# Kernel tuning notes

Measured on AMD Instinct MI355X. Metric: run time of the kernel, lower is better.

Reference implementation:

```python
import jax, jax.numpy as jnp
import numpy as np

T = 2048
HID = 4096
H = 32
HKV = 8
D = 128
EPS = 1e-5
THETA = 1e6
WINDOW = 1024


def setup_inputs() -> dict:
    key = jax.random.key(0)
    k1, k2, k3 = jax.random.split(key, 3)
    return {
        "positions": jnp.arange(T, dtype=jnp.int32),
        "hidden_states": jax.random.normal(k1, (T, HID), dtype=jnp.float32),
        "w_qkv": jax.random.normal(k2, (HID, (H + 2 * HKV) * D), dtype=jnp.float32) * 0.02,
        "q_norm_w": jnp.ones((D,), dtype=jnp.float32),
        "k_norm_w": jnp.ones((D,), dtype=jnp.float32),
        "w_o": jax.random.normal(k3, (H * D, HID), dtype=jnp.float32) * 0.02,
    }


def _rmsnorm(x, w):
    # per-head RMSNorm over last dim (head_dim)
    var = jnp.mean(x * x, axis=-1, keepdims=True)
    return x * jax.lax.rsqrt(var + EPS) * w


def _rope_neox(x, positions):
    # x: [T, heads, D]; neox style: rotate halves
    half = D // 2
    inv_freq = 1.0 / (THETA ** (jnp.arange(0, half, dtype=jnp.float32) / half))
    ang = positions.astype(jnp.float32)[:, None] * inv_freq  # [T, half]
    cos = jnp.cos(ang)[:, None, :]
    sin = jnp.sin(ang)[:, None, :]
    x1, x2 = x[..., :half], x[..., half:]
    return jnp.concatenate([x1 * cos - x2 * sin, x2 * cos + x1 * sin], axis=-1)


def reference(positions, hidden_states, w_qkv, q_norm_w, k_norm_w, w_o):
    qkv = hidden_states @ w_qkv  # [T, (H+2Hkv)*D]
    q, k, v = jnp.split(qkv, [H * D, (H + HKV) * D], axis=-1)
    q = _rmsnorm(q.reshape(T, H, D), q_norm_w)
    k = _rmsnorm(k.reshape(T, HKV, D), k_norm_w)
    v = v.reshape(T, HKV, D)

    q = _rope_neox(q, positions)
    k = _rope_neox(k, positions)

    # GQA: expand kv heads to H
    rep = H // HKV
    k = jnp.repeat(k, rep, axis=1)  # [T, H, D]
    v = jnp.repeat(v, rep, axis=1)

    scale = D ** -0.5
    scores = jnp.einsum('thd,shd->hts', q, k) * scale  # [H, T, T]
    i = jnp.arange(T)[:, None]
    j = jnp.arange(T)[None, :]
    mask = (j <= i) & (i - j < WINDOW)  # causal + sliding window
    scores = jnp.where(mask[None], scores, -jnp.inf)
    probs = jax.nn.softmax(scores, axis=-1)
    attn = jnp.einsum('hts,shd->thd', probs, v).reshape(T, H * D)
    return attn @ w_o
```

## Files before the change

kernel.cpp:

```cpp
#include <hip/hip_runtime.h>
#include <hip/hip_bf16.h>
#include <stdint.h>

#define T_SEQ  2048
#define HIDDEN 4096
#define NHEAD  32
#define NKV    8
#define HDIM   128
#define NQKV   6144
#define WINDOW 1024
#define SCALE  0.08838834764831845f
#define SHIFT  12.0f

typedef __attribute__((ext_vector_type(8))) short          short8;
typedef __attribute__((ext_vector_type(8))) unsigned short ushort8_t;
typedef __attribute__((ext_vector_type(4))) float          floatx4;

__device__ __forceinline__ unsigned short f2bf(float f) {
    union { float f; unsigned int u; } v; v.f = f;
    unsigned int u = v.u;
    unsigned int r = (u + 0x7FFFu + ((u >> 16) & 1u)) >> 16;
    return (unsigned short)r;
}
__device__ __forceinline__ float bf2f(unsigned short u) {
    union { unsigned int u; float f; } v; v.u = ((unsigned int)u) << 16;
    return v.f;
}

#define GLOBAL_AS(p) ((const __attribute__((address_space(1))) void*)(p))
#define LDS_AS(p)    ((__attribute__((address_space(3))) void*)(p))

#define S_BARRIER() do { asm volatile("" ::: "memory");  \
                         __builtin_amdgcn_s_barrier();   \
                         asm volatile("" ::: "memory"); } while (0)

__global__ __launch_bounds__(256) void convert_bf16_kernel(
        const float* __restrict__ X, unsigned short* __restrict__ Y, int n4) {
    int i = blockIdx.x * blockDim.x + threadIdx.x;
    if (i < n4) {
        float4 v = ((const float4*)X)[i];
        ushort4 o;
        o.x = f2bf(v.x); o.y = f2bf(v.y); o.z = f2bf(v.z); o.w = f2bf(v.w);
        ((ushort4*)Y)[i] = o;
    }
}

__global__ __launch_bounds__(256) void transpose_bf16_kernel(
        const float* __restrict__ W, unsigned short* __restrict__ Wt, int K, int N) {
    __shared__ float tile[128][33];
    const int n0 = blockIdx.x * 32, k0 = blockIdx.y * 128;
    const int tid = threadIdx.x;
    const int rr = tid >> 3, cc = tid & 7;
    #pragma unroll
    for (int p = 0; p < 4; ++p) {
        int r = p * 32 + rr;
        float4 v = *(const float4*)&W[(size_t)(k0 + r) * N + n0 + cc * 4];
        tile[r][cc * 4 + 0] = v.x; tile[r][cc * 4 + 1] = v.y;
        tile[r][cc * 4 + 2] = v.z; tile[r][cc * 4 + 3] = v.w;
    }
    __syncthreads();
    const int nL = tid >> 3, kc = tid & 7;
    #pragma unroll
    for (int q = 0; q < 2; ++q) {
        int kbase = kc * 8 + q * 64;
        ushort8_t o;
        #pragma unroll
        for (int j = 0; j < 8; ++j) o[j] = f2bf(tile[kbase + j][nL]);
        *(ushort8_t*)&Wt[(size_t)(n0 + nL) * K + k0 + kbase] = o;
    }
}

#define STG3_A(bufi, kt, r)                                                       \
    __builtin_amdgcn_global_load_lds(                                             \
        GLOBAL_AS(A + (size_t)(m0 + rRow[r]) * K + ((kt) << 6) + rOff[r]),        \
        LDS_AS(&As3[bufi][((r) * 256 + tid) * 8]), 16, 0, 0)
#define STG3_B(bufi, kt, r)                                                       \
    __builtin_amdgcn_global_load_lds(                                             \
        GLOBAL_AS(B + (size_t)(n0 + rRow[r]) * K + ((kt) << 6) + rOff[r]),        \
        LDS_AS(&Bs3[bufi][((r) * 256 + tid) * 8]), 16, 0, 0)

template <bool BF16_OUT>
__global__ __launch_bounds__(256, 2) void gemm_bt3_kernel(
        const unsigned short* __restrict__ A,
        const unsigned short* __restrict__ B,
        void* __restrict__ Cv, int M, int N, int K) {
    __shared__ __align__(16) unsigned short As3[2][128 * 64];
    __shared__ __align__(16) unsigned short Bs3[2][128 * 64];

    const int tid  = threadIdx.x;
    const int lane = tid & 63, wave = tid >> 6;
    const int wr = wave >> 1, wc = wave & 1;
    const int lrow = lane & 15, hi = lane >> 4;

    const int nwg = gridDim.x * gridDim.y;
    int wg = blockIdx.y * gridDim.x + blockIdx.x;
    wg = (wg & 7) * (nwg >> 3) + (wg >> 3);
    const int bx = wg % gridDim.x;
    const int by = wg / gridDim.x;
    const int m0 = by * 128, n0 = bx * 128;

    const int NT = K >> 6;

    int rRow[4], rOff[4];
    #pragma unroll
    for (int r = 0; r < 4; ++r) {
        int idx = r * 256 + tid;
        int row = idx >> 3;
        rRow[r] = row;
        rOff[r] = ((idx & 7) ^ (row & 7)) * 8;
    }

    const int sA0   = (hi ^ (lrow & 7)) * 8;
    const int aBase = (wr * 64 + lrow) * 64;
    const int bBase = (wc * 64 + lrow) * 64;

    floatx4 acc[4][4] = {};

    auto compute_tile = [&](int cur) {
        const unsigned short* ap = &As3[cur][0];
        const unsigned short* bp = &Bs3[cur][0];
        short8 af[4][2], bf[4][2];
        #pragma unroll
        for (int m = 0; m < 4; ++m)
            #pragma unroll
            for (int kh = 0; kh < 2; ++kh)
                af[m][kh] = *(const short8*)(ap + aBase + m * 1024 + (sA0 ^ (kh << 5)));
        #pragma unroll
        for (int n = 0; n < 4; ++n)
            #pragma unroll
            for (int kh = 0; kh < 2; ++kh)
                bf[n][kh] = *(const short8*)(bp + bBase + n * 1024 + (sA0 ^ (kh << 5)));
        __builtin_amdgcn_s_setprio(1);
        #pragma unroll
        for (int m = 0; m < 4; ++m)
            #pragma unroll
            for (int n = 0; n < 4; ++n) {
                acc[m][n] = __builtin_amdgcn_mfma_f32_16x16x32_bf16(
                    af[m][0], bf[n][0], acc[m][n], 0, 0, 0);
                acc[m][n] = __builtin_amdgcn_mfma_f32_16x16x32_bf16(
                    af[m][1], bf[n][1], acc[m][n], 0, 0, 0);
            }
        __builtin_amdgcn_s_setprio(0);
    };

    #pragma unroll
    for (int r = 0; r < 4; ++r) STG3_A(0, 0, r);
    #pragma unroll
    for (int r = 0; r < 4; ++r) STG3_B(0, 0, r);
    asm volatile("s_waitcnt vmcnt(0)" ::: "memory");
    S_BARRIER();

    for (int t = 0; t < NT - 1; ++t) {
        const int cur = t & 1;
        #pragma unroll
        for (int r = 0; r < 4; ++r) STG3_A(cur ^ 1, t + 1, r);
        #pragma unroll
        for (int r = 0; r < 4; ++r) STG3_B(cur ^ 1, t + 1, r);
        compute_tile(cur);
        asm volatile("s_waitcnt vmcnt(0)" ::: "memory");
        S_BARRIER();
    }
    compute_tile((NT - 1) & 1);

    const int rowb = hi * 4, col = lrow;
    #pragma unroll
    for (int mi = 0; mi < 4; ++mi)
        #pragma unroll
        for (int ni = 0; ni < 4; ++ni) {
            size_t base = (size_t)(m0 + wr * 64 + mi * 16 + rowb) * N
                        + (n0 + wc * 64 + ni * 16 + col);
            #pragma unroll
            for (int r = 0; r < 4; ++r) {
                if (BF16_OUT)
                    ((unsigned short*)Cv)[base + (size_t)r * N] = f2bf(acc[mi][ni][r]);
                else
                    ((float*)Cv)[base + (size_t)r * N] = acc[mi][ni][r];
            }
        }
}

#define STG4_A(bufi, kt, r)                                                       \
    __builtin_amdgcn_global_load_lds(                                             \
        GLOBAL_AS(A + (size_t)(m0 + rRowA[r]) * K + ((kt) << 6) + rOffA[r]),      \
        LDS_AS(&As4[bufi][((r) * 256 + tid) * 8]), 16, 0, 0)
#define STG4_B(bufi, kt, r)                                                       \
    __builtin_amdgcn_global_load_lds(                                             \
        GLOBAL_AS(B + (size_t)(n0 + rRowB[r]) * K + ((kt) << 6) + rOffB[r]),      \
        LDS_AS(&Bs4[bufi][((r) * 256 + tid) * 8]), 16, 0, 0)

template <bool BF16_OUT>
__global__ __launch_bounds__(256, 2) void gemm_bt4_kernel(
        const unsigned short* __restrict__ A,
        const unsigned short* __restrict__ B,
        void* __restrict__ Cv, int M, int N, int K) {
    __shared__ __align__(16) unsigned short As4[2][128 * 64];
    __shared__ __align__(16) unsigned short Bs4[2][192 * 64];

    const int tid  = threadIdx.x;
    const int lane = tid & 63, wave = tid >> 6;
    const int wr = wave >> 1, wc = wave & 1;
    const int lrow = lane & 15, hi = lane >> 4;

    const int nwg = gridDim.x * gridDim.y;
    int wg = blockIdx.y * gridDim.x + blockIdx.x;
    wg = (wg & 7) * (nwg >> 3) + (wg >> 3);
    const int by = wg % gridDim.x;
    const int bx = wg / gridDim.x;
    const int m0 = by * 128, n0 = bx * 192;

    const int NT = K >> 6;

    int rRowA[4], rOffA[4];
    #pragma unroll
    for (int r = 0; r < 4; ++r) {
        int idx = r * 256 + tid;
        int row = idx >> 3;
        rRowA[r] = row;
        rOffA[r] = ((idx & 7) ^ (row & 7)) * 8;
    }
    int rRowB[6], rOffB[6];
    #pragma unroll
    for (int r = 0; r < 6; ++r) {
        int idx = r * 256 + tid;
        int row = idx >> 3;
        rRowB[r] = row;
        rOffB[r] = ((idx & 7) ^ (row & 7)) * 8;
    }

    const int sA0   = (hi ^ (lrow & 7)) * 8;
    const int aBase = (wr * 64 + lrow) * 64;
    const int bBase = (wc * 96 + lrow) * 64;

    floatx4 acc[4][6] = {};

    auto compute_tile = [&](int cur) {
        const unsigned short* ap = &As4[cur][0];
        const unsigned short* bp = &Bs4[cur][0];
        short8 af[4][2], bf[6][2];
        #pragma unroll
        for (int m = 0; m < 4; ++m)
            #pragma unroll
            for (int kh = 0; kh < 2; ++kh)
                af[m][kh] = *(const short8*)(ap + aBase + m * 1024 + (sA0 ^ (kh << 5)));
        #pragma unroll
        for (int n = 0; n < 6; ++n)
            #pragma unroll
            for (int kh = 0; kh < 2; ++kh)
                bf[n][kh] = *(const short8*)(bp + bBase + n * 1024 + (sA0 ^ (kh << 5)));
        __builtin_amdgcn_s_setprio(1);
        #pragma unroll
        for (int m = 0; m < 4; ++m)
            #pragma unroll
            for (int n = 0; n < 6; ++n) {
                acc[m][n] = __builtin_amdgcn_mfma_f32_16x16x32_bf16(
                    af[m][0], bf[n][0], acc[m][n], 0, 0, 0);
                acc[m][n] = __builtin_amdgcn_mfma_f32_16x16x32_bf16(
                    af[m][1], bf[n][1], acc[m][n], 0, 0, 0);
            }
        __builtin_amdgcn_s_setprio(0);
    };

    #pragma unroll
    for (int r = 0; r < 4; ++r) STG4_A(0, 0, r);
    #pragma unroll
    for (int r = 0; r < 6; ++r) STG4_B(0, 0, r);
    asm volatile("s_waitcnt vmcnt(0)" ::: "memory");
    S_BARRIER();

    for (int t = 0; t < NT - 1; ++t) {
        const int cur = t & 1;
        #pragma unroll
        for (int r = 0; r < 4; ++r) STG4_A(cur ^ 1, t + 1, r);
        #pragma unroll
        for (int r = 0; r < 6; ++r) STG4_B(cur ^ 1, t + 1, r);
        compute_tile(cur);
        asm volatile("s_waitcnt vmcnt(0)" ::: "memory");
        S_BARRIER();
    }
    compute_tile((NT - 1) & 1);

    const int rowb = hi * 4, col = lrow;
    #pragma unroll
    for (int mi = 0; mi < 4; ++mi)
        #pragma unroll
        for (int ni = 0; ni < 6; ++ni) {
            size_t base = (size_t)(m0 + wr * 64 + mi * 16 + rowb) * N
                        + (n0 + wc * 96 + ni * 16 + col);
            #pragma unroll
            for (int r = 0; r < 4; ++r) {
                if (BF16_OUT)
                    ((unsigned short*)Cv)[base + (size_t)r * N] = f2bf(acc[mi][ni][r]);
                else
                    ((float*)Cv)[base + (size_t)r * N] = acc[mi][ni][r];
            }
        }
}

__global__ __launch_bounds__(256) void rope_table_kernel(
        const int* __restrict__ positions, float2* __restrict__ rope) {
    int idx = blockIdx.x * 256 + threadIdx.x;
    int t = idx >> 6, i = idx & 63;
    float inv_freq = expf((float)i * -0.2158673524681918f);
    float sn, cs;
    sincosf((float)positions[t] * inv_freq, &sn, &cs);
    rope[idx] = make_float2(cs, sn);
}

__global__ __launch_bounds__(256) void qkv_post_kernel(
        const unsigned short* __restrict__ qkv, const float2* __restrict__ rope,
        const float* __restrict__ qw, const float* __restrict__ kw,
        unsigned short* __restrict__ qb,
        unsigned short* __restrict__ kb,
        unsigned short* __restrict__ vbT) {
    const int head = blockIdx.y;
    const int t0   = blockIdx.x * 32;
    const int tid  = threadIdx.x;

    if (head < 40) {
        const int r  = tid >> 3;
        const int q8 = tid & 7;
        const int t  = t0 + r;
        const unsigned short* src = qkv + (size_t)t * NQKV
                         + (head < 32 ? head * 128 : 4096 + (head - 32) * 128)
                         + q8 * 16;
        const float* w = (head < 32) ? qw : kw;

        ushort8_t u0 = *(const ushort8_t*)src;
        ushort8_t u1 = *(const ushort8_t*)(src + 8);
        float x[16];
        #pragma unroll
        for (int j = 0; j < 8; ++j) { x[j] = bf2f(u0[j]); x[8 + j] = bf2f(u1[j]); }

        float ss = 0.f;
        #pragma unroll
        for (int j = 0; j < 16; ++j) ss = fmaf(x[j], x[j], ss);
        ss += __shfl_xor(ss, 1); ss += __shfl_xor(ss, 2); ss += __shfl_xor(ss, 4);
        float sc = rsqrtf(ss * (1.f / 128.f) + 1e-5f);

        float xn[16], xp[16];
        #pragma unroll
        for (int j = 0; j < 16; ++j) xn[j] = x[j] * sc * w[q8 * 16 + j];
        #pragma unroll
        for (int j = 0; j < 16; ++j) xp[j] = __shfl_xor(xn[j], 4);

        const float2* rp = rope + (size_t)t * 64 + (q8 & 3) * 16;
        ushort8_t o0, o1;
        #pragma unroll
        for (int j = 0; j < 8; ++j) {
            float2 cs = rp[j];
            float res = (q8 < 4) ? (xn[j] * cs.x - xp[j] * cs.y)
                                 : (xn[j] * cs.x + xp[j] * cs.y);
            o0[j] = f2bf(res);
        }
        #pragma unroll
        for (int j = 0; j < 8; ++j) {
            float2 cs = rp[8 + j];
            float res = (q8 < 4) ? (xn[8+j] * cs.x - xp[8+j] * cs.y)
                                 : (xn[8+j] * cs.x + xp[8+j] * cs.y);
            o1[j] = f2bf(res);
        }
        unsigned short* dst = (head < 32)
            ? qb + ((size_t)t * 32 + head) * 128 + q8 * 16
            : kb + ((size_t)t * 8 + (head - 32)) * 128 + q8 * 16;
        *(ushort8_t*)dst       = o0;
        *(ushort8_t*)(dst + 8) = o1;
    } else {
        __shared__ float tile[128][33];
        const int hk = head - 40;
        {
            const int r = tid >> 3, c8 = tid & 7;
            const unsigned short* src =
                qkv + (size_t)(t0 + r) * NQKV + 5120 + hk * 128 + c8 * 16;
            ushort8_t u0 = *(const ushort8_t*)src;
            ushort8_t u1 = *(const ushort8_t*)(src + 8);
            #pragma unroll
            for (int j = 0; j < 8; ++j) {
                tile[c8 * 16 + j][r]     = bf2f(u0[j]);
                tile[c8 * 16 + 8 + j][r] = bf2f(u1[j]);
            }
        }
        __syncthreads();
        {
            const int d = tid >> 1, th = tid & 1;
            ushort8_t o0, o1;
            #pragma unroll
            for (int j = 0; j < 8; ++j) o0[j] = f2bf(tile[d][th * 16 + j]);
            #pragma unroll
            for (int j = 0; j < 8; ++j) o1[j] = f2bf(tile[d][th * 16 + 8 + j]);
            unsigned short* dst = vbT + ((size_t)hk * 128 + d) * T_SEQ + t0 + th * 16;
            *(ushort8_t*)dst       = o0;
            *(ushort8_t*)(dst + 8) = o1;
        }
    }
}

__global__ __launch_bounds__(256) void attention_kernel(
        const unsigned short* __restrict__ qb,
        const unsigned short* __restrict__ kb,
        const unsigned short* __restrict__ vbT,
        unsigned short* __restrict__ attnb) {
    const int h    = blockIdx.x & 31;
    const int Q0   = (blockIdx.x >> 5) * 64;
    const int tid  = threadIdx.x, wave = tid >> 6, lane = tid & 63;
    const int keyA = lane & 15, g = lane >> 4;
    const int hk   = h >> 2;
    const int qlo  = Q0 + wave * 16;

    __shared__ __align__(16) unsigned short ks [2][32 * 128];
    __shared__ __align__(16) unsigned short vsT[2][128 * 32];
    __shared__ __align__(16) unsigned short Pa [4 * 16 * 40];

    unsigned short* pw = Pa + wave * 640;

    int kRow[2], kOff[2], vD[2], vOff[2];
    #pragma unroll
    for (int i = 0; i < 2; ++i) {
        int c = i * 256 + tid;
        {   int row = c >> 4, u = c & 15;
            kRow[i] = row; kOff[i] = (u ^ (row & 7)) * 8; }
        {   int d = c >> 2, u = c & 3;
            vD[i] = d; vOff[i] = (u ^ (d & 3)) * 8; }
    }

    auto stage = [&](int buf, int s0) {
        #pragma unroll
        for (int i = 0; i < 2; ++i) {
            int c = i * 256 + tid;
            const unsigned short* kp =
                kb + ((size_t)(s0 + kRow[i]) * 8 + hk) * 128 + kOff[i];
            __builtin_amdgcn_global_load_lds(GLOBAL_AS(kp),
                LDS_AS(&ks[buf][c * 8]), 16, 0, 0);
            const unsigned short* vp =
                vbT + ((size_t)hk * 128 + vD[i]) * T_SEQ + s0 + vOff[i];
            __builtin_amdgcn_global_load_lds(GLOBAL_AS(vp),
                LDS_AS(&vsT[buf][c * 8]), 16, 0, 0);
        }
    };

    short8 qa[4];
    {
        const unsigned short* qp = qb + ((size_t)(qlo + keyA) * 32 + h) * 128 + g * 8;
        #pragma unroll
        for (int s = 0; s < 4; ++s) qa[s] = *(const short8*)(qp + s * 32);
    }

    floatx4 acc[8] = {};
    float l_part[4] = {0.f, 0.f, 0.f, 0.f};

    const int s_begin = (Q0 >= WINDOW) ? ((Q0 - (WINDOW - 1)) & ~31) : 0;
    const int s_end   = Q0 + 63;

    stage(0, s_begin);
    asm volatile("s_waitcnt vmcnt(0)" ::: "memory");
    S_BARRIER();

    int cur = 0;
    for (int s0 = s_begin; s0 <= s_end; s0 += 32) {
        if (s0 + 32 <= s_end) stage(cur ^ 1, s0 + 32);

        if (s0 <= qlo + 15 && s0 + 31 >= qlo - (WINDOW - 1)) {
            const unsigned short* ksb  = &ks[cur][0];
            const unsigned short* vsb  = &vsT[cur][0];
            floatx4 sa0 = {}, sa1 = {};
            #pragma unroll
            for (int kst = 0; kst < 4; ++kst) {
                int u = g + 4 * kst;
                short8 k0 = *(const short8*)(ksb + keyA * 128 + (u ^ (keyA & 7)) * 8);
                short8 k1 = *(const short8*)(ksb + (16 + keyA) * 128 + (u ^ ((16 + keyA) & 7)) * 8);
                sa0 = __builtin_amdgcn_mfma_f32_16x16x32_bf16(qa[kst], k0, sa0, 0, 0, 0);
                sa1 = __builtin_amdgcn_mfma_f32_16x16x32_bf16(qa[kst], k1, sa1, 0, 0, 0);
            }
            float p0[4], p1[4];
            #pragma unroll
            for (int r = 0; r < 4; ++r) {
                int row = qlo + 4 * g + r;
                int sA = s0 + keyA, sB = sA + 16;
                bool vA = (sA <= row) && (row - sA < WINDOW);
                bool vB = (sB <= row) && (row - sB < WINDOW);
                p0[r] = vA ? __expf(fmaf(sa0[r], SCALE, -SHIFT)) : 0.f;
                p1[r] = vB ? __expf(fmaf(sa1[r], SCALE, -SHIFT)) : 0.f;
                l_part[r] += p0[r] + p1[r];
            }
            #pragma unroll
            for (int r = 0; r < 4; ++r) {
                pw[(4 * g + r) * 40 + keyA]      = f2bf(p0[r]);
                pw[(4 * g + r) * 40 + keyA + 16] = f2bf(p1[r]);
            }
            short8 pf = *(const short8*)(pw + keyA * 40 + g * 8);

            #pragma unroll
            for (int t = 0; t < 8; ++t) {
                int d = t * 16 + keyA;
                short8 vf = *(const short8*)(vsb + d * 32 + (g ^ (d & 3)) * 8);
                acc[t] = __builtin_amdgcn_mfma_f32_16x16x32_bf16(pf, vf, acc[t], 0, 0, 0);
            }
        }
        asm volatile("s_waitcnt vmcnt(0)" ::: "memory");
        S_BARRIER();
        cur ^= 1;
    }

    float inv[4];
    #pragma unroll
    for (int r = 0; r < 4; ++r) {
        float l = l_part[r];
        l += __shfl_xor(l, 1); l += __shfl_xor(l, 2);
        l += __shfl_xor(l, 4); l += __shfl_xor(l, 8);
        inv[r] = 1.f / l;
    }
    #pragma unroll
    for (int t = 0; t < 8; ++t)
        #pragma unroll
        for (int r = 0; r < 4; ++r)
            attnb[(size_t)(qlo + 4 * g + r) * 4096 + h * 128 + t * 16 + keyA] =
                f2bf(acc[t][r] * inv[r]);
}

extern "C" void kernel_launch(void* const* d_in, const int* in_sizes, int n_in,
                              void* d_out, int out_size, void* d_ws, size_t ws_size,
                              hipStream_t stream) {
    const int*   positions = (const int*)  d_in[0];
    const float* hs        = (const float*)d_in[1];
    const float* w_qkv     = (const float*)d_in[2];
    const float* q_norm_w  = (const float*)d_in[3];
    const float* k_norm_w  = (const float*)d_in[4];
    const float* w_o       = (const float*)d_in[5];
    float* out = (float*)d_out;

    char* ws = (char*)d_ws;
    unsigned short* hsb   = (unsigned short*)(ws);
    unsigned short* wqkvt = (unsigned short*)(ws + (size_t)(16u << 20));
    unsigned short* wot   = (unsigned short*)(ws + (size_t)(64u << 20));
    unsigned short* qkvb  = (unsigned short*)(ws + (size_t)(96u << 20));
    unsigned short* qb    = (unsigned short*)(ws + (size_t)(16u << 20));
    unsigned short* kb    = (unsigned short*)(ws + (size_t)(32u << 20));
    unsigned short* vbT   = (unsigned short*)(ws + (size_t)(36u << 20));
    float2*         rope  = (float2*)        (ws + (size_t)(40u << 20));
    unsigned short* attnb = hsb;

    convert_bf16_kernel<<<dim3((T_SEQ * HIDDEN / 4 + 255) / 256), 256, 0, stream>>>(
        hs, hsb, T_SEQ * HIDDEN / 4);
    transpose_bf16_kernel<<<dim3(NQKV / 32, HIDDEN / 128), 256, 0, stream>>>(
        w_qkv, wqkvt, HIDDEN, NQKV);
    transpose_bf16_kernel<<<dim3(HIDDEN / 32, HIDDEN / 128), 256, 0, stream>>>(
        w_o, wot, HIDDEN, HIDDEN);
    gemm_bt4_kernel<true><<<dim3(T_SEQ / 128, NQKV / 192), 256, 0, stream>>>(
        hsb, wqkvt, qkvb, T_SEQ, NQKV, HIDDEN);
    rope_table_kernel<<<dim3(T_SEQ * 64 / 256), 256, 0, stream>>>(positions, rope);
    qkv_post_kernel<<<dim3(T_SEQ / 32, 48), 256, 0, stream>>>(
        qkvb, rope, q_norm_w, k_norm_w, qb, kb, vbT);
    attention_kernel<<<dim3((T_SEQ / 64) * NHEAD), 256, 0, stream>>>(
        qb, kb, vbT, attnb);
    gemm_bt3_kernel<false><<<dim3(HIDDEN / 128, T_SEQ / 128), 256, 0, stream>>>(
        attnb, wot, out, T_SEQ, HIDDEN, HIDDEN);
}
```

Measured before the change: 505.6 us.

## Prefetch two K-tiles ahead in GEMM kernels with partial vmcnt waits

Result: faster. 488.1 us (-3.5%).

```diff
diff --git a/kernel.cpp b/kernel.cpp
--- a/kernel.cpp
+++ b/kernel.cpp
@@ -116,7 +116,7 @@
 
     floatx4 acc[4][4] = {};
 
-    auto compute_tile = [&](int cur) {
+    auto kstep = [&](int cur, int t2, int mode) {
         const unsigned short* ap = &As3[cur][0];
         const unsigned short* bp = &Bs3[cur][0];
         short8 af[4][2], bf[4][2];
@@ -130,6 +130,15 @@
             #pragma unroll
             for (int kh = 0; kh < 2; ++kh)
                 bf[n][kh] = *(const short8*)(bp + bBase + n * 1024 + (sA0 ^ (kh << 5)));
+        asm volatile("s_waitcnt lgkmcnt(0)" ::: "memory");
+        __builtin_amdgcn_s_barrier();
+        asm volatile("" ::: "memory");
+        if (mode == 0) {
+            #pragma unroll
+            for (int r = 0; r < 4; ++r) STG3_A(cur, t2, r);
+            #pragma unroll
+            for (int r = 0; r < 4; ++r) STG3_B(cur, t2, r);
+        }
         __builtin_amdgcn_s_setprio(1);
         #pragma unroll
         for (int m = 0; m < 4; ++m)
@@ -141,26 +150,32 @@
                     af[m][1], bf[n][1], acc[m][n], 0, 0, 0);
             }
         __builtin_amdgcn_s_setprio(0);
+        if (mode == 0) {
+            asm volatile("s_waitcnt vmcnt(8)" ::: "memory");
+            __builtin_amdgcn_s_barrier();
+            asm volatile("" ::: "memory");
+        } else if (mode == 1) {
+            asm volatile("s_waitcnt vmcnt(0)" ::: "memory");
+            __builtin_amdgcn_s_barrier();
+            asm volatile("" ::: "memory");
+        }
     };
 
     #pragma unroll
     for (int r = 0; r < 4; ++r) STG3_A(0, 0, r);
     #pragma unroll
     for (int r = 0; r < 4; ++r) STG3_B(0, 0, r);
-    asm volatile("s_waitcnt vmcnt(0)" ::: "memory");
+    #pragma unroll
+    for (int r = 0; r < 4; ++r) STG3_A(1, 1, r);
+    #pragma unroll
+    for (int r = 0; r < 4; ++r) STG3_B(1, 1, r);
+    asm volatile("s_waitcnt vmcnt(8)" ::: "memory");
     S_BARRIER();
 
-    for (int t = 0; t < NT - 1; ++t) {
-        const int cur = t & 1;
-        #pragma unroll
-        for (int r = 0; r < 4; ++r) STG3_A(cur ^ 1, t + 1, r);
-        #pragma unroll
-        for (int r = 0; r < 4; ++r) STG3_B(cur ^ 1, t + 1, r);
-        compute_tile(cur);
-        asm volatile("s_waitcnt vmcnt(0)" ::: "memory");
-        S_BARRIER();
-    }
-    compute_tile((NT - 1) & 1);
+    int t = 0;
+    for (; t < NT - 2; ++t) kstep(t & 1, t + 2, 0);
+    kstep(t & 1, 0, 1); ++t;
+    kstep(t & 1, 0, 2);
 
     const int rowb = hi * 4, col = lrow;
     #pragma unroll
@@ -233,7 +248,7 @@
 
     floatx4 acc[4][6] = {};
 
-    auto compute_tile = [&](int cur) {
+    auto kstep = [&](int cur, int t2, int mode) {
         const unsigned short* ap = &As4[cur][0];
         const unsigned short* bp = &Bs4[cur][0];
         short8 af[4][2], bf[6][2];
@@ -247,6 +262,15 @@
             #pragma unroll
             for (int kh = 0; kh < 2; ++kh)
                 bf[n][kh] = *(const short8*)(bp + bBase + n * 1024 + (sA0 ^ (kh << 5)));
+        asm volatile("s_waitcnt lgkmcnt(0)" ::: "memory");
+        __builtin_amdgcn_s_barrier();
+        asm volatile("" ::: "memory");
+        if (mode == 0) {
+            #pragma unroll
+            for (int r = 0; r < 4; ++r) STG4_A(cur, t2, r);
+            #pragma unroll
+            for (int r = 0; r < 6; ++r) STG4_B(cur, t2, r);
+        }
         __builtin_amdgcn_s_setprio(1);
         #pragma unroll
         for (int m = 0; m < 4; ++m)
@@ -258,26 +282,32 @@
                     af[m][1], bf[n][1], acc[m][n], 0, 0, 0);
             }
         __builtin_amdgcn_s_setprio(0);
+        if (mode == 0) {
+            asm volatile("s_waitcnt vmcnt(10)" ::: "memory");
+            __builtin_amdgcn_s_barrier();
+            asm volatile("" ::: "memory");
+        } else if (mode == 1) {
+            asm volatile("s_waitcnt vmcnt(0)" ::: "memory");
+            __builtin_amdgcn_s_barrier();
+            asm volatile("" ::: "memory");
+        }
     };
 
     #pragma unroll
     for (int r = 0; r < 4; ++r) STG4_A(0, 0, r);
     #pragma unroll
     for (int r = 0; r < 6; ++r) STG4_B(0, 0, r);
-    asm volatile("s_waitcnt vmcnt(0)" ::: "memory");
+    #pragma unroll
+    for (int r = 0; r < 4; ++r) STG4_A(1, 1, r);
+    #pragma unroll
+    for (int r = 0; r < 6; ++r) STG4_B(1, 1, r);
+    asm volatile("s_waitcnt vmcnt(10)" ::: "memory");
     S_BARRIER();
 
-    for (int t = 0; t < NT - 1; ++t) {
-        const int cur = t & 1;
-        #pragma unroll
-        for (int r = 0; r < 4; ++r) STG4_A(cur ^ 1, t + 1, r);
-        #pragma unroll
-        for (int r = 0; r < 6; ++r) STG4_B(cur ^ 1, t + 1, r);
-        compute_tile(cur);
-        asm volatile("s_waitcnt vmcnt(0)" ::: "memory");
-        S_BARRIER();
-    }
-    compute_tile((NT - 1) & 1);
+    int t = 0;
+    for (; t < NT - 2; ++t) kstep(t & 1, t + 2, 0);
+    kstep(t & 1, 0, 1); ++t;
+    kstep(t & 1, 0, 2);
 
     const int rowb = hi * 4, col = lrow;
     #pragma unroll
```
